# Optimization experiments

Measured on AMD Instinct MI355X. Metric: run time of the kernel, lower is better.

The kernel has to match this reference:

```python
import jax, jax.numpy as jnp
from jax import lax
import numpy as np

HIDDEN = 512
NUM_LAYERS = 2
NUM_KEYS = 128
BATCH = 256
SEQ = 512


def setup_inputs() -> dict:
    key = jax.random.key(0)
    ks = jax.random.split(key, 16)
    s = 0.05  # keep gates out of saturation
    inp = {
        "x": jax.random.normal(ks[0], (BATCH, SEQ, NUM_KEYS), dtype=jnp.float32),
        # layer 0 (input size NUM_KEYS); PyTorch gate order i,f,g,o stacked on dim0
        "W_ih0": jax.random.normal(ks[1], (4 * HIDDEN, NUM_KEYS), dtype=jnp.float32) * s,
        "W_hh0": jax.random.normal(ks[2], (4 * HIDDEN, HIDDEN), dtype=jnp.float32) * s,
        "b_ih0": jax.random.normal(ks[3], (4 * HIDDEN,), dtype=jnp.float32) * s,
        "b_hh0": jax.random.normal(ks[4], (4 * HIDDEN,), dtype=jnp.float32) * s,
        # layer 1 (input size HIDDEN)
        "W_ih1": jax.random.normal(ks[5], (4 * HIDDEN, HIDDEN), dtype=jnp.float32) * s,
        "W_hh1": jax.random.normal(ks[6], (4 * HIDDEN, HIDDEN), dtype=jnp.float32) * s,
        "b_ih1": jax.random.normal(ks[7], (4 * HIDDEN,), dtype=jnp.float32) * s,
        "b_hh1": jax.random.normal(ks[8], (4 * HIDDEN,), dtype=jnp.float32) * s,
        # final linear head
        "W_fc": jax.random.normal(ks[9], (NUM_KEYS, HIDDEN), dtype=jnp.float32) * s,
        "b_fc": jax.random.normal(ks[10], (NUM_KEYS,), dtype=jnp.float32) * s,
    }
    return inp


def _lstm_layer(xs, W_ih, W_hh, b_ih, b_hh):
    # xs: [B, T, in]. Precompute input contribution to all gates outside the scan.
    B = xs.shape[0]
    H = W_hh.shape[1]
    xg = jnp.einsum("bti,gi->btg", xs, W_ih) + b_ih + b_hh  # [B, T, 4H]

    def step(carry, xg_t):
        h, c = carry
        g = xg_t + h @ W_hh.T  # [B, 4H]
        i, f, gg, o = jnp.split(g, 4, axis=-1)
        i = jax.nn.sigmoid(i)
        f = jax.nn.sigmoid(f)
        gg = jnp.tanh(gg)
        o = jax.nn.sigmoid(o)
        c = f * c + i * gg
        h = o * jnp.tanh(c)
        return (h, c), h

    h0 = jnp.zeros((B, H), xs.dtype)
    (_, _), hs = lax.scan(step, (h0, h0), jnp.swapaxes(xg, 0, 1))  # hs: [T, B, H]
    return jnp.swapaxes(hs, 0, 1)  # [B, T, H]


def reference(x, W_ih0, W_hh0, b_ih0, b_hh0, W_ih1, W_hh1, b_ih1, b_hh1, W_fc, b_fc):
    h = _lstm_layer(x, W_ih0, W_hh0, b_ih0, b_hh0)
    h = _lstm_layer(h, W_ih1, W_hh1, b_ih1, b_hh1)
    return h[:, -1, :] @ W_fc.T + b_fc  # [B, NUM_KEYS]
```

## Files before the change

kernel.cpp:

```cpp
#include <hip/hip_runtime.h>

#define HIDDEN 512
#define TSEQ 512
#define NKEYS 128

typedef short short8_t __attribute__((ext_vector_type(8)));
typedef short short4_t __attribute__((ext_vector_type(4)));
typedef float f32x4 __attribute__((ext_vector_type(4)));
typedef int i32x4 __attribute__((ext_vector_type(4)));

__device__ __forceinline__ ushort f2bf(float f) {
    union { float f; unsigned u; } v; v.f = f;
    unsigned r = (v.u + 0x7FFFu + ((v.u >> 16) & 1u)) >> 16;
    return (ushort)r;
}
__device__ __forceinline__ float sigm(float x) { return 1.0f / (1.0f + __expf(-x)); }
__device__ __forceinline__ float tanh_f(float x) { return 2.0f / (1.0f + __expf(-2.0f * x)) - 1.0f; }

__global__ void cast_w(const float* __restrict__ Wih, const float* __restrict__ Whh,
                       ushort* __restrict__ Wc, int KIN, int K) {
    long idx = (long)blockIdx.x * blockDim.x + threadIdx.x;
    if (idx >= (long)2048 * K) return;
    int row = (int)(idx / K), k = (int)(idx % K);
    float v = (k < KIN) ? Wih[(long)row * KIN + k] : Whh[(long)row * HIDDEN + (k - KIN)];
    Wc[idx] = f2bf(v);
}

__global__ void prep_bias(const float* __restrict__ a, const float* __restrict__ b,
                          const float* __restrict__ c, const float* __restrict__ d,
                          float* __restrict__ b0, float* __restrict__ b1) {
    int i = blockIdx.x * blockDim.x + threadIdx.x;
    if (i < 2048) { b0[i] = a[i] + b[i]; b1[i] = c[i] + d[i]; }
}

__global__ void init_zeros(ushort* __restrict__ h0buf, ushort* __restrict__ h1par) {
    int idx = blockIdx.x * blockDim.x + threadIdx.x;
    ushort4 z = {0, 0, 0, 0};
    if (idx < 32768) {
        int b = idx >> 7, off = (idx & 127) * 4;
        *(ushort4*)(h0buf + (size_t)b * 513 * 512 + off) = z;
    } else {
        int j = idx - 32768;
        *(ushort4*)(h1par + (size_t)j * 4) = z;
    }
}

#define AF_LIST_20(M) M(0)M(1)M(2)M(3)M(4)M(5)M(6)M(7)M(8)M(9)M(10)M(11)M(12)M(13)M(14)M(15)M(16)M(17)M(18)M(19)
#define AF_LIST_32(M) AF_LIST_20(M) M(20)M(21)M(22)M(23)M(24)M(25)M(26)M(27)M(28)M(29)M(30)M(31)

#define AF_DECL(i) short8_t af##i;
#define AF_LOAD(i) af##i = *(const short8_t*)(wsrc + (i) * 32); \
                   asm volatile("" : "+a"(af##i));

#define AF_MFMA(i) { \
    const char* _b  = ((i) < KSI) ? (bpi + (i) * 64) : (bpr + ((i) - KSI) * 64); \
    const int   _r16 = ((i) < KSI) ? (16 * INROW) : (16 * RECROW); \
    short8_t bf0 = *(const short8_t*)_b; \
    short8_t bf1 = *(const short8_t*)(_b + _r16); \
    if ((i) & 1) { \
        asm("v_mfma_f32_16x16x32_bf16 %0, %1, %2, %0" : "+v"(accA1) : "a"(af##i), "v"(bf0)); \
        asm("v_mfma_f32_16x16x32_bf16 %0, %1, %2, %0" : "+v"(accB1) : "a"(af##i), "v"(bf1)); \
    } else { \
        asm("v_mfma_f32_16x16x32_bf16 %0, %1, %2, %0" : "+v"(accA0) : "a"(af##i), "v"(bf0)); \
        asm("v_mfma_f32_16x16x32_bf16 %0, %1, %2, %0" : "+v"(accB0) : "a"(af##i), "v"(bf1)); \
    } }

template <int L>
__device__ __forceinline__ void lstm_body(
    char* smem, int bid,
    const float* __restrict__ x, const ushort* __restrict__ Wc,
    const float* __restrict__ biasc, ushort* __restrict__ h0buf,
    ushort* __restrict__ h1par, float* __restrict__ hlast, int* flags)
{
    constexpr int KIN   = L ? 512 : 128;
    constexpr int K     = KIN + 512;
    constexpr int KSI   = KIN / 32;
    constexpr int INROW = L ? 1056 : 288;
    constexpr int RECROW = 1056;
    constexpr int RECPAR = 32 * RECROW;
    constexpr size_t RST0 = 513 * 512;

    char* const recb = smem;
    char* const inb  = smem + 2 * RECPAR;

    const int tid = threadIdx.x;
    const int tile = bid & 7;
    const int g    = (bid >> 3) & 15;
    const int b0   = tile * 32;
    const int w = tid >> 6, lane = tid & 63, hi4 = lane >> 4, arow = lane & 15;
    const int Uw = g * 32 + w * 4;
    const int row_l = 512 * (arow & 3) + Uw + (arow >> 2);

    int* const ownbase  = flags + (L ? 4096 : 0) + tile * 512;
    int* const prodbase = flags + tile * 512;
    int* const myflag   = ownbase + g * 32;

    AF_LIST_32(AF_DECL)
    {
        const ushort* wsrc = Wc + (size_t)row_l * K + hi4 * 8;
        if constexpr (L == 0) { AF_LIST_20(AF_LOAD) }
        else                  { AF_LIST_32(AF_LOAD) }
    }
    f32x4 bias4;
#pragma unroll
    for (int r = 0; r < 4; ++r) bias4[r] = biasc[512 * r + Uw + hi4];

    for (int i = tid; i < 2 * RECPAR / 4; i += 512) ((int*)recb)[i] = 0;

    float c0 = 0.0f, c1 = 0.0f;

    const int si = tid >> 4, sj = tid & 15;
    float4 xa, xb;
    if constexpr (L == 0) {
        const float* xp = x + ((size_t)(b0 + si) * TSEQ) * NKEYS + sj * 8;
        xa = *(const float4*)xp; xb = *(const float4*)(xp + 4);
    }

    const bool notown = (lane >> 2) != g;
    const int* pollp; int thrOff;
    if constexpr (L == 0) {
        pollp = ownbase + (lane & 15) * 32;
        thrOff = ((lane & 15) == g) ? -0x100000 : 0;
    } else {
        const int prod = (lane >> 4) & 1;
        pollp = (prod ? prodbase : ownbase) + (lane & 15) * 32;
        thrOff = prod ? 1 : (((lane & 15) == g) ? -0x100000 : 0);
    }

    __syncthreads();

#pragma unroll 1
    for (int t = 0; t < TSEQ; ++t) {
        const int par = t & 1;
        char* const rb_cur = recb + par * RECPAR;
        char* const rb_nxt = recb + (par ^ 1) * RECPAR;

        if constexpr (L == 0) {
            short8_t s;
            s[0] = (short)f2bf(xa.x); s[1] = (short)f2bf(xa.y);
            s[2] = (short)f2bf(xa.z); s[3] = (short)f2bf(xa.w);
            s[4] = (short)f2bf(xb.x); s[5] = (short)f2bf(xb.y);
            s[6] = (short)f2bf(xb.z); s[7] = (short)f2bf(xb.w);
            *(short8_t*)(inb + si * INROW + sj * 16) = s;
        }

        {
            const int thr = t + thrOff;
            while (true) {
                int v;
                asm volatile("global_load_dword %0, %1, off sc0 sc1\n\t"
                             "s_waitcnt vmcnt(0)"
                             : "=&v"(v) : "v"((unsigned long long)pollp) : "memory");
                if (__all(v >= thr)) break;
                __builtin_amdgcn_s_sleep(1);
            }
        }

        {
            i32x4 q0, q1, q2, q3;
            if constexpr (L == 1) {
                const ushort* ib = h0buf + ((size_t)(b0 + w * 4) * 513 + (t + 1)) * 512 + lane * 8;
                asm volatile("global_load_dwordx4 %0, %4, off sc0 sc1\n\t"
                             "global_load_dwordx4 %1, %5, off sc0 sc1\n\t"
                             "global_load_dwordx4 %2, %6, off sc0 sc1\n\t"
                             "global_load_dwordx4 %3, %7, off sc0 sc1"
                             : "=&v"(q0), "=&v"(q1), "=&v"(q2), "=&v"(q3)
                             : "v"((unsigned long long)ib),
                               "v"((unsigned long long)(ib + RST0)),
                               "v"((unsigned long long)(ib + 2 * RST0)),
                               "v"((unsigned long long)(ib + 3 * RST0))
                             : "memory");
            }
            i32x4 r0, r1, r2, r3;
            if (notown) {
                const ushort* rb;
                size_t rstr;
                if constexpr (L == 0) {
                    rb = h0buf + ((size_t)(b0 + w * 4) * 513 + t) * 512 + lane * 8;
                    rstr = RST0;
                } else {
                    rb = h1par + ((size_t)(par * 256) + b0 + w * 4) * 512 + lane * 8;
                    rstr = 512;
                }
                asm volatile("global_load_dwordx4 %0, %4, off sc0 sc1\n\t"
                             "global_load_dwordx4 %1, %5, off sc0 sc1\n\t"
                             "global_load_dwordx4 %2, %6, off sc0 sc1\n\t"
                             "global_load_dwordx4 %3, %7, off sc0 sc1"
                             : "=&v"(r0), "=&v"(r1), "=&v"(r2), "=&v"(r3)
                             : "v"((unsigned long long)rb),
                               "v"((unsigned long long)(rb + rstr)),
                               "v"((unsigned long long)(rb + 2 * rstr)),
                               "v"((unsigned long long)(rb + 3 * rstr))
                             : "memory");
            }
            asm volatile("s_waitcnt vmcnt(0)" ::: "memory");
            if constexpr (L == 1) {
                *(i32x4*)(inb + (w * 4 + 0) * INROW + lane * 16) = q0;
                *(i32x4*)(inb + (w * 4 + 1) * INROW + lane * 16) = q1;
                *(i32x4*)(inb + (w * 4 + 2) * INROW + lane * 16) = q2;
                *(i32x4*)(inb + (w * 4 + 3) * INROW + lane * 16) = q3;
            }
            if (notown) {
                *(i32x4*)(rb_cur + (w * 4 + 0) * RECROW + lane * 16) = r0;
                *(i32x4*)(rb_cur + (w * 4 + 1) * RECROW + lane * 16) = r1;
                *(i32x4*)(rb_cur + (w * 4 + 2) * RECROW + lane * 16) = r2;
                *(i32x4*)(rb_cur + (w * 4 + 3) * RECROW + lane * 16) = r3;
            }
        }
        if constexpr (L == 0) {
            const int tt = (t + 1) & 511;
            const float* xp = x + ((size_t)(b0 + si) * TSEQ + tt) * NKEYS + sj * 8;
            xa = *(const float4*)xp; xb = *(const float4*)(xp + 4);
        }
        __syncthreads();

        f32x4 accA0 = bias4, accB0 = bias4;
        f32x4 accA1 = {0.f, 0.f, 0.f, 0.f}, accB1 = {0.f, 0.f, 0.f, 0.f};
        const char* bpi = inb + arow * INROW + hi4 * 16;
        const char* bpr = rb_cur + arow * RECROW + hi4 * 16;
        if constexpr (L == 0) { AF_LIST_20(AF_MFMA) }
        else                  { AF_LIST_32(AF_MFMA) }
        asm volatile("s_nop 7\n\ts_nop 7"
                     : "+v"(accA0), "+v"(accA1), "+v"(accB0), "+v"(accB1));
        f32x4 am0 = accA0 + accA1, am1 = accB0 + accB1;

        float ig0 = sigm(am0[0]), fg0 = sigm(am0[1]);
        float gg0 = tanh_f(am0[2]), og0 = sigm(am0[3]);
        c0 = fg0 * c0 + ig0 * gg0;
        float h0f = og0 * tanh_f(c0);
        float ig1 = sigm(am1[0]), fg1 = sigm(am1[1]);
        float gg1 = tanh_f(am1[2]), og1 = sigm(am1[3]);
        c1 = fg1 * c1 + ig1 * gg1;
        float h1f = og1 * tanh_f(c1);
        int hv0 = f2bf(h0f), hv1 = f2bf(h1f);

        *(ushort*)(rb_nxt + arow * RECROW + (Uw + hi4) * 2)        = (ushort)hv0;
        *(ushort*)(rb_nxt + (16 + arow) * RECROW + (Uw + hi4) * 2) = (ushort)hv1;

        int a0 = __shfl(hv0, arow, 64),      a1 = __shfl(hv0, 16 + arow, 64);
        int a2 = __shfl(hv0, 32 + arow, 64), a3 = __shfl(hv0, 48 + arow, 64);
        int e0 = __shfl(hv1, arow, 64),      e1 = __shfl(hv1, 16 + arow, 64);
        int e2 = __shfl(hv1, 32 + arow, 64), e3 = __shfl(hv1, 48 + arow, 64);
        if (hi4 == 0) {
            unsigned lo0 = (a0 & 0xFFFF) | (a1 << 16);
            unsigned hi0 = (a2 & 0xFFFF) | (a3 << 16);
            unsigned long long pk0 = lo0 | ((unsigned long long)hi0 << 32);
            unsigned lo1 = (e0 & 0xFFFF) | (e1 << 16);
            unsigned hi1 = (e2 & 0xFFFF) | (e3 << 16);
            unsigned long long pk1 = lo1 | ((unsigned long long)hi1 << 32);
            const ushort* d0;
            const ushort* d1;
            if constexpr (L == 0) {
                d0 = h0buf + ((size_t)(b0 + arow) * 513 + (t + 1)) * 512 + Uw;
                d1 = h0buf + ((size_t)(b0 + 16 + arow) * 513 + (t + 1)) * 512 + Uw;
            } else {
                const size_t pr = (size_t)((t + 1) & 1) * 256;
                d0 = h1par + (pr + b0 + arow) * 512 + Uw;
                d1 = h1par + (pr + b0 + 16 + arow) * 512 + Uw;
            }
            asm volatile("global_store_dwordx2 %0, %2, off sc0 sc1\n\t"
                         "global_store_dwordx2 %1, %3, off sc0 sc1"
                         :: "v"((unsigned long long)d0), "v"((unsigned long long)d1),
                            "v"(pk0), "v"(pk1) : "memory");
        }
        if (L == 1 && t == TSEQ - 1) {
            hlast[(size_t)(b0 + arow) * 512 + Uw + hi4]      = h0f;
            hlast[(size_t)(b0 + 16 + arow) * 512 + Uw + hi4] = h1f;
        }

        asm volatile("s_waitcnt vmcnt(0)" ::: "memory");
        __syncthreads();
        if (tid == 0)
            asm volatile("global_store_dword %0, %1, off sc0 sc1"
                         :: "v"((unsigned long long)myflag), "v"(t + 1) : "memory");
    }
}

__global__ __attribute__((amdgpu_waves_per_eu(2, 2))) __launch_bounds__(512)
void lstm_fused(const float* __restrict__ x,
                const ushort* __restrict__ Wc0, const ushort* __restrict__ Wc1,
                const float* __restrict__ bg0, const float* __restrict__ bg1,
                ushort* __restrict__ h0buf, ushort* __restrict__ h1par,
                float* __restrict__ hlast, int* flags)
{
    __shared__ __align__(16) char smem[101376];
    const int bid = blockIdx.x;
    if (bid < 128) lstm_body<0>(smem, bid, x, Wc0, bg0, h0buf, h1par, hlast, flags);
    else           lstm_body<1>(smem, bid, x, Wc1, bg1, h0buf, h1par, hlast, flags);
}

__global__ void fc_kernel(const float* __restrict__ hlast, const float* __restrict__ Wfc,
                          const float* __restrict__ bfc, float* __restrict__ out) {
    __shared__ float hs[HIDDEN];
    const int b = blockIdx.x, n = threadIdx.x;
    for (int k = n; k < HIDDEN; k += 128) hs[k] = hlast[b * HIDDEN + k];
    __syncthreads();
    const float* wr = Wfc + (long)n * HIDDEN;
    float acc = bfc[n];
#pragma unroll 8
    for (int k = 0; k < HIDDEN; ++k) acc += hs[k] * wr[k];
    out[b * 128 + n] = acc;
}

extern "C" void kernel_launch(void* const* d_in, const int* in_sizes, int n_in,
                              void* d_out, int out_size, void* d_ws, size_t ws_size,
                              hipStream_t stream) {
    const float* x    = (const float*)d_in[0];
    const float* Wih0 = (const float*)d_in[1];
    const float* Whh0 = (const float*)d_in[2];
    const float* bih0 = (const float*)d_in[3];
    const float* bhh0 = (const float*)d_in[4];
    const float* Wih1 = (const float*)d_in[5];
    const float* Whh1 = (const float*)d_in[6];
    const float* bih1 = (const float*)d_in[7];
    const float* bhh1 = (const float*)d_in[8];
    const float* Wfc  = (const float*)d_in[9];
    const float* bfc  = (const float*)d_in[10];

    char* ws = (char*)d_ws;
    size_t off = 0;
    auto alloc = [&](size_t bytes) {
        void* p = ws + off;
        off = (off + bytes + 255) & ~(size_t)255;
        return p;
    };
    ushort* Wc0   = (ushort*)alloc(2048UL * 640 * 2);
    ushort* Wc1   = (ushort*)alloc(2048UL * 1024 * 2);
    float*  bg0   = (float*)alloc(2048 * 4);
    float*  bg1   = (float*)alloc(2048 * 4);
    float*  hlast = (float*)alloc(256UL * 512 * 4);
    ushort* h1par = (ushort*)alloc(2UL * 256 * 512 * 2);
    int*    flags = (int*)alloc(65536);
    ushort* h0buf = (ushort*)alloc(256UL * 513 * 512 * 2);
    if (ws_size < off) return;

    hipMemsetAsync(flags, 0, 65536, stream);
    init_zeros<<<256, 256, 0, stream>>>(h0buf, h1par);
    cast_w<<<(2048 * 640  + 255) / 256, 256, 0, stream>>>(Wih0, Whh0, Wc0, 128, 640);
    cast_w<<<(2048 * 1024 + 255) / 256, 256, 0, stream>>>(Wih1, Whh1, Wc1, 512, 1024);
    prep_bias<<<8, 256, 0, stream>>>(bih0, bhh0, bih1, bhh1, bg0, bg1);

    {
        void* args[] = { (void*)&x, (void*)&Wc0, (void*)&Wc1, (void*)&bg0, (void*)&bg1,
                         (void*)&h0buf, (void*)&h1par, (void*)&hlast, (void*)&flags };
        hipLaunchCooperativeKernel((const void*)lstm_fused, dim3(256), dim3(512),
                                   args, 0, stream);
    }

    fc_kernel<<<256, 128, 0, stream>>>(hlast, Wfc, bfc, (float*)d_out);
}
```

Measured before the change: 2.183 ms.

## Re-layout hidden-state exchange buffers into per-publisher contiguous chunks with staged LDS stores

Reorganizes the global h buffers so each producer block's 32x32 hidden slice sits in one contiguous 2KB chunk per timestep. Producers now write their slice from LDS after the barrier with wide dwordx4 stores from one wave, replacing shuffle-packed dwordx2 stores. Consumers read these contiguous chunks, and layer-1 input reads of h0 switch to plain cached loads. The aim is fewer, more coalesced cross-block transfers on the recurrent critical path. In exchange, wave 0 serializes the publish step, and the cached loads depend on the flag protocol for correctness.

```diff
diff --git a/kernel.cpp b/kernel.cpp
--- a/kernel.cpp
+++ b/kernel.cpp
@@ -33,16 +33,11 @@
     if (i < 2048) { b0[i] = a[i] + b[i]; b1[i] = c[i] + d[i]; }
 }
 
-__global__ void init_zeros(ushort* __restrict__ h0buf, ushort* __restrict__ h1par) {
+__global__ void init_zeros(ushort* __restrict__ h0s, ushort* __restrict__ h1p) {
     int idx = blockIdx.x * blockDim.x + threadIdx.x;
     ushort4 z = {0, 0, 0, 0};
-    if (idx < 32768) {
-        int b = idx >> 7, off = (idx & 127) * 4;
-        *(ushort4*)(h0buf + (size_t)b * 513 * 512 + off) = z;
-    } else {
-        int j = idx - 32768;
-        *(ushort4*)(h1par + (size_t)j * 4) = z;
-    }
+    if (idx < 32768) *(ushort4*)(h0s + (size_t)idx * 4) = z;
+    else             *(ushort4*)(h1p + (size_t)(idx - 32768) * 4) = z;
 }
 
 #define AF_LIST_20(M) M(0)M(1)M(2)M(3)M(4)M(5)M(6)M(7)M(8)M(9)M(10)M(11)M(12)M(13)M(14)M(15)M(16)M(17)M(18)M(19)
@@ -69,8 +64,8 @@
 __device__ __forceinline__ void lstm_body(
     char* smem, int bid,
     const float* __restrict__ x, const ushort* __restrict__ Wc,
-    const float* __restrict__ biasc, ushort* __restrict__ h0buf,
-    ushort* __restrict__ h1par, float* __restrict__ hlast, int* flags)
+    const float* __restrict__ biasc, ushort* __restrict__ h0s,
+    ushort* __restrict__ h1p, float* __restrict__ hlast, int* flags)
 {
     constexpr int KIN   = L ? 512 : 128;
     constexpr int K     = KIN + 512;
@@ -78,7 +73,7 @@
     constexpr int INROW = L ? 1056 : 288;
     constexpr int RECROW = 1056;
     constexpr int RECPAR = 32 * RECROW;
-    constexpr size_t RST0 = 513 * 512;
+    constexpr size_t TSTR = 128 * 1024;
 
     char* const recb = smem;
     char* const inb  = smem + 2 * RECPAR;
@@ -116,7 +111,8 @@
         xa = *(const float4*)xp; xb = *(const float4*)(xp + 4);
     }
 
-    const bool notown = (lane >> 2) != g;
+    const int pub = lane >> 2, q = lane & 3;
+    const bool notown = pub != g;
     const int* pollp; int thrOff;
     if constexpr (L == 0) {
         pollp = ownbase + (lane & 15) * 32;
@@ -157,54 +153,51 @@
         }
 
         {
-            i32x4 q0, q1, q2, q3;
+            i32x4 i0, i1, i2, i3;
             if constexpr (L == 1) {
-                const ushort* ib = h0buf + ((size_t)(b0 + w * 4) * 513 + (t + 1)) * 512 + lane * 8;
-                asm volatile("global_load_dwordx4 %0, %4, off sc0 sc1\n\t"
-                             "global_load_dwordx4 %1, %5, off sc0 sc1\n\t"
-                             "global_load_dwordx4 %2, %6, off sc0 sc1\n\t"
-                             "global_load_dwordx4 %3, %7, off sc0 sc1"
-                             : "=&v"(q0), "=&v"(q1), "=&v"(q2), "=&v"(q3)
-                             : "v"((unsigned long long)ib),
-                               "v"((unsigned long long)(ib + RST0)),
-                               "v"((unsigned long long)(ib + 2 * RST0)),
-                               "v"((unsigned long long)(ib + 3 * RST0))
-                             : "memory");
+                const ushort* ib = h0s + ((size_t)(t + 1)) * TSTR
+                                   + ((size_t)tile * 16 + pub) * 1024 + (size_t)w * 128 + q * 8;
+                i0 = *(const i32x4*)(ib);
+                i1 = *(const i32x4*)(ib + 32);
+                i2 = *(const i32x4*)(ib + 64);
+                i3 = *(const i32x4*)(ib + 96);
             }
             i32x4 r0, r1, r2, r3;
             if (notown) {
-                const ushort* rb;
-                size_t rstr;
                 if constexpr (L == 0) {
-                    rb = h0buf + ((size_t)(b0 + w * 4) * 513 + t) * 512 + lane * 8;
-                    rstr = RST0;
+                    const ushort* rb = h0s + ((size_t)t) * TSTR
+                                       + ((size_t)tile * 16 + pub) * 1024 + (size_t)w * 128 + q * 8;
+                    r0 = *(const i32x4*)(rb);
+                    r1 = *(const i32x4*)(rb + 32);
+                    r2 = *(const i32x4*)(rb + 64);
+                    r3 = *(const i32x4*)(rb + 96);
                 } else {
-                    rb = h1par + ((size_t)(par * 256) + b0 + w * 4) * 512 + lane * 8;
-                    rstr = 512;
+                    const ushort* rb = h1p + (((size_t)par * 8 + tile) * 16 + pub) * 1024
+                                       + (size_t)w * 128 + q * 8;
+                    asm volatile("global_load_dwordx4 %0, %4, off sc0 sc1\n\t"
+                                 "global_load_dwordx4 %1, %5, off sc0 sc1\n\t"
+                                 "global_load_dwordx4 %2, %6, off sc0 sc1\n\t"
+                                 "global_load_dwordx4 %3, %7, off sc0 sc1\n\t"
+                                 "s_waitcnt vmcnt(0)"
+                                 : "=&v"(r0), "=&v"(r1), "=&v"(r2), "=&v"(r3)
+                                 : "v"((unsigned long long)rb),
+                                   "v"((unsigned long long)(rb + 32)),
+                                   "v"((unsigned long long)(rb + 64)),
+                                   "v"((unsigned long long)(rb + 96))
+                                 : "memory");
                 }
-                asm volatile("global_load_dwordx4 %0, %4, off sc0 sc1\n\t"
-                             "global_load_dwordx4 %1, %5, off sc0 sc1\n\t"
-                             "global_load_dwordx4 %2, %6, off sc0 sc1\n\t"
-                             "global_load_dwordx4 %3, %7, off sc0 sc1"
-                             : "=&v"(r0), "=&v"(r1), "=&v"(r2), "=&v"(r3)
-                             : "v"((unsigned long long)rb),
-                               "v"((unsigned long long)(rb + rstr)),
-                               "v"((unsigned long long)(rb + 2 * rstr)),
-                               "v"((unsigned long long)(rb + 3 * rstr))
-                             : "memory");
-            }
-            asm volatile("s_waitcnt vmcnt(0)" ::: "memory");
+            }
             if constexpr (L == 1) {
-                *(i32x4*)(inb + (w * 4 + 0) * INROW + lane * 16) = q0;
-                *(i32x4*)(inb + (w * 4 + 1) * INROW + lane * 16) = q1;
-                *(i32x4*)(inb + (w * 4 + 2) * INROW + lane * 16) = q2;
-                *(i32x4*)(inb + (w * 4 + 3) * INROW + lane * 16) = q3;
+                *(i32x4*)(inb + (w * 4 + 0) * INROW + pub * 64 + q * 16) = i0;
+                *(i32x4*)(inb + (w * 4 + 1) * INROW + pub * 64 + q * 16) = i1;
+                *(i32x4*)(inb + (w * 4 + 2) * INROW + pub * 64 + q * 16) = i2;
+                *(i32x4*)(inb + (w * 4 + 3) * INROW + pub * 64 + q * 16) = i3;
             }
             if (notown) {
-                *(i32x4*)(rb_cur + (w * 4 + 0) * RECROW + lane * 16) = r0;
-                *(i32x4*)(rb_cur + (w * 4 + 1) * RECROW + lane * 16) = r1;
-                *(i32x4*)(rb_cur + (w * 4 + 2) * RECROW + lane * 16) = r2;
-                *(i32x4*)(rb_cur + (w * 4 + 3) * RECROW + lane * 16) = r3;
+                *(i32x4*)(rb_cur + (w * 4 + 0) * RECROW + pub * 64 + q * 16) = r0;
+                *(i32x4*)(rb_cur + (w * 4 + 1) * RECROW + pub * 64 + q * 16) = r1;
+                *(i32x4*)(rb_cur + (w * 4 + 2) * RECROW + pub * 64 + q * 16) = r2;
+                *(i32x4*)(rb_cur + (w * 4 + 3) * RECROW + pub * 64 + q * 16) = r3;
             }
         }
         if constexpr (L == 0) {
@@ -232,47 +225,35 @@
         float gg1 = tanh_f(am1[2]), og1 = sigm(am1[3]);
         c1 = fg1 * c1 + ig1 * gg1;
         float h1f = og1 * tanh_f(c1);
-        int hv0 = f2bf(h0f), hv1 = f2bf(h1f);
-
-        *(ushort*)(rb_nxt + arow * RECROW + (Uw + hi4) * 2)        = (ushort)hv0;
-        *(ushort*)(rb_nxt + (16 + arow) * RECROW + (Uw + hi4) * 2) = (ushort)hv1;
-
-        int a0 = __shfl(hv0, arow, 64),      a1 = __shfl(hv0, 16 + arow, 64);
-        int a2 = __shfl(hv0, 32 + arow, 64), a3 = __shfl(hv0, 48 + arow, 64);
-        int e0 = __shfl(hv1, arow, 64),      e1 = __shfl(hv1, 16 + arow, 64);
-        int e2 = __shfl(hv1, 32 + arow, 64), e3 = __shfl(hv1, 48 + arow, 64);
-        if (hi4 == 0) {
-            unsigned lo0 = (a0 & 0xFFFF) | (a1 << 16);
-            unsigned hi0 = (a2 & 0xFFFF) | (a3 << 16);
-            unsigned long long pk0 = lo0 | ((unsigned long long)hi0 << 32);
-            unsigned lo1 = (e0 & 0xFFFF) | (e1 << 16);
-            unsigned hi1 = (e2 & 0xFFFF) | (e3 << 16);
-            unsigned long long pk1 = lo1 | ((unsigned long long)hi1 << 32);
-            const ushort* d0;
-            const ushort* d1;
-            if constexpr (L == 0) {
-                d0 = h0buf + ((size_t)(b0 + arow) * 513 + (t + 1)) * 512 + Uw;
-                d1 = h0buf + ((size_t)(b0 + 16 + arow) * 513 + (t + 1)) * 512 + Uw;
-            } else {
-                const size_t pr = (size_t)((t + 1) & 1) * 256;
-                d0 = h1par + (pr + b0 + arow) * 512 + Uw;
-                d1 = h1par + (pr + b0 + 16 + arow) * 512 + Uw;
-            }
-            asm volatile("global_store_dwordx2 %0, %2, off sc0 sc1\n\t"
-                         "global_store_dwordx2 %1, %3, off sc0 sc1"
-                         :: "v"((unsigned long long)d0), "v"((unsigned long long)d1),
-                            "v"(pk0), "v"(pk1) : "memory");
-        }
+
+        *(ushort*)(rb_nxt + arow * RECROW + (Uw + hi4) * 2)        = (ushort)f2bf(h0f);
+        *(ushort*)(rb_nxt + (16 + arow) * RECROW + (Uw + hi4) * 2) = (ushort)f2bf(h1f);
         if (L == 1 && t == TSEQ - 1) {
             hlast[(size_t)(b0 + arow) * 512 + Uw + hi4]      = h0f;
             hlast[(size_t)(b0 + 16 + arow) * 512 + Uw + hi4] = h1f;
         }
 
-        asm volatile("s_waitcnt vmcnt(0)" ::: "memory");
         __syncthreads();
-        if (tid == 0)
-            asm volatile("global_store_dword %0, %1, off sc0 sc1"
-                         :: "v"((unsigned long long)myflag), "v"(t + 1) : "memory");
+
+        if (w == 0) {
+            ushort* dst;
+            if constexpr (L == 0)
+                dst = h0s + ((size_t)(t + 1)) * TSTR + ((size_t)tile * 16 + g) * 1024;
+            else
+                dst = h1p + (((size_t)((t + 1) & 1) * 8 + tile) * 16 + g) * 1024;
+#pragma unroll
+            for (int k = 0; k < 2; ++k) {
+                const int row = k * 16 + (lane >> 2);
+                i32x4 d = *(const i32x4*)(rb_nxt + row * RECROW + g * 64 + (lane & 3) * 16);
+                asm volatile("global_store_dwordx4 %0, %1, off sc0 sc1"
+                             :: "v"((unsigned long long)(dst + row * 32 + (lane & 3) * 8)),
+                                "v"(d) : "memory");
+            }
+            asm volatile("s_waitcnt vmcnt(0)" ::: "memory");
+            if (tid == 0)
+                asm volatile("global_store_dword %0, %1, off sc0 sc1"
+                             :: "v"((unsigned long long)myflag), "v"(t + 1) : "memory");
+        }
     }
 }
 
@@ -280,13 +261,13 @@
 void lstm_fused(const float* __restrict__ x,
                 const ushort* __restrict__ Wc0, const ushort* __restrict__ Wc1,
                 const float* __restrict__ bg0, const float* __restrict__ bg1,
-                ushort* __restrict__ h0buf, ushort* __restrict__ h1par,
+                ushort* __restrict__ h0s, ushort* __restrict__ h1p,
                 float* __restrict__ hlast, int* flags)
 {
     __shared__ __align__(16) char smem[101376];
     const int bid = blockIdx.x;
-    if (bid < 128) lstm_body<0>(smem, bid, x, Wc0, bg0, h0buf, h1par, hlast, flags);
-    else           lstm_body<1>(smem, bid, x, Wc1, bg1, h0buf, h1par, hlast, flags);
+    if (bid < 128) lstm_body<0>(smem, bid, x, Wc0, bg0, h0s, h1p, hlast, flags);
+    else           lstm_body<1>(smem, bid, x, Wc1, bg1, h0s, h1p, hlast, flags);
 }
 
 __global__ void fc_kernel(const float* __restrict__ hlast, const float* __restrict__ Wfc,
@@ -329,20 +310,20 @@
     float*  bg0   = (float*)alloc(2048 * 4);
     float*  bg1   = (float*)alloc(2048 * 4);
     float*  hlast = (float*)alloc(256UL * 512 * 4);
-    ushort* h1par = (ushort*)alloc(2UL * 256 * 512 * 2);
+    ushort* h1p   = (ushort*)alloc(2UL * 128 * 1024 * 2);
     int*    flags = (int*)alloc(65536);
-    ushort* h0buf = (ushort*)alloc(256UL * 513 * 512 * 2);
+    ushort* h0s   = (ushort*)alloc(513UL * 128 * 1024 * 2);
     if (ws_size < off) return;
 
     hipMemsetAsync(flags, 0, 65536, stream);
-    init_zeros<<<256, 256, 0, stream>>>(h0buf, h1par);
+    init_zeros<<<256, 256, 0, stream>>>(h0s, h1p);
     cast_w<<<(2048 * 640  + 255) / 256, 256, 0, stream>>>(Wih0, Whh0, Wc0, 128, 640);
     cast_w<<<(2048 * 1024 + 255) / 256, 256, 0, stream>>>(Wih1, Whh1, Wc1, 512, 1024);
     prep_bias<<<8, 256, 0, stream>>>(bih0, bhh0, bih1, bhh1, bg0, bg1);
 
     {
         void* args[] = { (void*)&x, (void*)&Wc0, (void*)&Wc1, (void*)&bg0, (void*)&bg1,
-                         (void*)&h0buf, (void*)&h1par, (void*)&hlast, (void*)&flags };
+                         (void*)&h0s, (void*)&h1p, (void*)&hlast, (void*)&flags };
         hipLaunchCooperativeKernel((const void*)lstm_fused, dim3(256), dim3(512),
                                    args, 0, stream);
     }
```

Result: slower. 2.485 ms (+13.8%).
